# Optimization experiments

Measured on AMD Instinct MI355X. Metric: run time of the kernel, lower is better.

Reference implementation:

```python
import jax, jax.numpy as jnp
import numpy as np

T = 48; S = 48; H = 250; EMB = 300; VOCAB = 50000; NL = 5


def setup_inputs():
    key = jax.random.key(0)
    ks = jax.random.split(key, 32)
    def rn(k, shape, scale=0.05):
        return jax.random.normal(k, shape, dtype=jnp.float32) * scale
    return {
        "x1": jax.random.randint(ks[0], (T,), 0, VOCAB),
        "x2": jax.random.randint(ks[1], (S,), 0, VOCAB),
        "emb": rn(ks[2], (VOCAB, EMB), 1.0),
        "w_ih_f": rn(ks[3], (4 * H, EMB)),
        "w_hh_f": rn(ks[4], (4 * H, H)),
        "b_f": rn(ks[5], (4 * H,)),
        "w_ih_b": rn(ks[6], (4 * H, EMB)),
        "w_hh_b": rn(ks[7], (4 * H, H)),
        "b_b": rn(ks[8], (4 * H,)),
        "c1_w": rn(ks[9], (128, 13, 3, 3)),  "c1_b": rn(ks[10], (128,)),
        "c2_w": rn(ks[11], (164, 128, 3, 3)), "c2_b": rn(ks[12], (164,)),
        "c3_w": rn(ks[13], (192, 164, 3, 3)), "c3_b": rn(ks[14], (192,)),
        "c4_w": rn(ks[15], (192, 192, 3, 3)), "c4_b": rn(ks[16], (192,)),
        "c5_w": rn(ks[17], (128, 192, 3, 3)), "c5_b": rn(ks[18], (128,)),
        "dnn_w": rn(ks[19], (128, 128)), "dnn_b": rn(ks[20], (128,)),
        "out_w": rn(ks[21], (NL, 128)), "out_b": rn(ks[22], (NL,)),
    }


def _lstm_dir(xW, w_hh, b, reverse):
    # xW: [T, 4H] precomputed input projection
    def cell(carry, g_in):
        h, c = carry
        g = g_in + h @ w_hh.T + b
        i, f, gg, o = jnp.split(g, 4)
        i = jax.nn.sigmoid(i); f = jax.nn.sigmoid(f)
        gg = jnp.tanh(gg); o = jax.nn.sigmoid(o)
        c = f * c + i * gg
        h = o * jnp.tanh(c)
        return (h, c), h
    h0 = jnp.zeros((w_hh.shape[1],), xW.dtype)
    _, hs = jax.lax.scan(cell, (h0, h0), xW, reverse=reverse)
    return hs  # [T, H], aligned to input positions


def _bilstm(x, w_ih_f, w_hh_f, b_f, w_ih_b, w_hh_b, b_b):
    hf = _lstm_dir(x @ w_ih_f.T, w_hh_f, b_f, False)
    hb = _lstm_dir(x @ w_ih_b.T, w_hh_b, b_b, True)
    return jnp.stack([hf, hb], axis=1)  # [T, 2, H]


def _sim(a, b):
    # a:[T,D], b:[S,D] -> [3,T,S] channels (dot, cos, l2) -- fully batched
    dot = a @ b.T
    na = jnp.sqrt(jnp.sum(a * a, -1))
    nb = jnp.sqrt(jnp.sum(b * b, -1))
    cos = dot / (na[:, None] * nb[None, :] + 1e-8)
    d2 = jnp.maximum(na[:, None] ** 2 + nb[None, :] ** 2 - 2.0 * dot, 1e-12)
    l2 = jnp.sqrt(d2)
    return jnp.stack([dot, cos, l2], 0)


def _sim_cube(seq1, seq2):
    h1f, h1b = seq1[:, 0], seq1[:, 1]
    h2f, h2b = seq2[:, 0], seq2[:, 1]
    parts = [
        _sim(jnp.concatenate([h1f, h1b], -1), jnp.concatenate([h2f, h2b], -1)),
        _sim(h1f, h2f),
        _sim(h1b, h2b),
        _sim(h1f + h1b, h2f + h2b),
    ]
    pad = jnp.zeros((1, seq1.shape[0], seq2.shape[0]), seq1.dtype)  # channel 12
    return jnp.concatenate(parts + [pad], 0)  # [13, T, S]


def _greedy_select(plane):
    # greedy non-conflicting pair selection over top (T+S) entries
    t, s = plane.shape
    _, idx = jax.lax.top_k(plane.reshape(-1), t + s)
    def step(carry, i):
        s1, s2, m = carry
        p1 = i // t  # faithful to original (divides by len(s1tag))
        p2 = i % s
        ok = (s1[p1] + s2[p2]) == 0
        s1 = s1.at[p1].set(jnp.where(ok, 1, s1[p1]))
        s2 = s2.at[p2].set(jnp.where(ok, 1, s2[p2]))
        m = m.at[p1, p2].set(m[p1, p2] | ok)
        return (s1, s2, m), None
    init = (jnp.zeros(t, jnp.int32), jnp.zeros(s, jnp.int32), jnp.zeros((t, s), bool))
    (_, _, m), _ = jax.lax.scan(step, init, idx)
    return m


def _focus_cube(sc):
    sel = _greedy_select(sc[10]) | _greedy_select(sc[11])
    mask = jnp.where(sel[None], 1.0, 0.1).astype(sc.dtype)  # 0.1 base per VDPWI
    mask = mask.at[12].set(1.0)
    return mask * sc


def _convnet(x, c1_w, c1_b, c2_w, c2_b, c3_w, c3_b, c4_w, c4_b, c5_w, c5_b,
             dnn_w, dnn_b, out_w, out_b):
    def conv(x, w, b):
        y = jax.lax.conv_general_dilated(
            x, w, (1, 1), ((1, 1), (1, 1)),
            dimension_numbers=("NCHW", "OIHW", "NCHW"))
        return y + b[None, :, None, None]
    def pool(x, k, st):
        return jax.lax.reduce_window(
            x, -jnp.inf, jax.lax.max, (1, 1, k, k), (1, 1, st, st), "VALID")
    x = pool(jax.nn.relu(conv(x, c1_w, c1_b)), 2, 2)  # 48->24
    x = pool(jax.nn.relu(conv(x, c2_w, c2_b)), 2, 2)  # 24->12
    x = pool(jax.nn.relu(conv(x, c3_w, c3_b)), 2, 2)  # 12->6
    x = pool(jax.nn.relu(conv(x, c4_w, c4_b)), 2, 2)  # 6->3
    x = pool(jax.nn.relu(conv(x, c5_w, c5_b)), 3, 1)  # 3->1
    x = x.reshape(x.shape[0], -1)  # [1, 128]
    x = jax.nn.relu(x @ dnn_w.T + dnn_b)
    return x @ out_w.T + out_b


def reference(x1, x2, emb, w_ih_f, w_hh_f, b_f, w_ih_b, w_hh_b, b_b,
              c1_w, c1_b, c2_w, c2_b, c3_w, c3_b, c4_w, c4_b, c5_w, c5_b,
              dnn_w, dnn_b, out_w, out_b):
    e1 = emb[x1]  # [T, 300]
    e2 = emb[x2]  # [S, 300]
    seq1 = _bilstm(e1, w_ih_f, w_hh_f, b_f, w_ih_b, w_hh_b, b_b)
    seq2 = _bilstm(e2, w_ih_f, w_hh_f, b_f, w_ih_b, w_hh_b, b_b)
    sc = _sim_cube(seq1, seq2)        # [13, T, S]
    fc = _focus_cube(sc)
    logits = _convnet(fc[None], c1_w, c1_b, c2_w, c2_b, c3_w, c3_b,
                      c4_w, c4_b, c5_w, c5_b, dnn_w, dnn_b, out_w, out_b)
    return jax.nn.log_softmax(logits, axis=-1)
```

## Files before the change

### kernel.cpp

```cpp
#include <hip/hip_runtime.h>
#include <math.h>


typedef __attribute__((ext_vector_type(2))) _Float16 h2f;
typedef unsigned long long u64;

#define OFF_XW    0
#define OFF_HS    192000
#define OFF_SC    240000
#define OFF_BUFA  269952
#define OFF_BUFB  343680
#define OFF_WIHT  367296
#define OFF_WPK   967296
#define OFF_SEL   1217296

__device__ __forceinline__ float sigf(float x) { return 1.f / (1.f + expf(-x)); }

#if __has_builtin(__builtin_amdgcn_fdot2)
__device__ __forceinline__ float dot2(h2f a, h2f b, float c) {
    return __builtin_amdgcn_fdot2(a, b, c, false);
}
#else
__device__ __forceinline__ float dot2(h2f a, h2f b, float c) {
    return c + (float)a.x * (float)b.x + (float)a.y * (float)b.y;
}
#endif

__global__ void transpose_wih_kernel(const float* __restrict__ wf, const float* __restrict__ wb,
                                     float* __restrict__ wT)
{
    __shared__ float tile[32][33];
    int dir = blockIdx.z;
    const float* w = dir ? wb : wf;

    int j = blockIdx.x * 32 + threadIdx.y;
    int k = blockIdx.y * 32 + threadIdx.x;
    if (j < 1000 && k < 300)
        tile[threadIdx.y][threadIdx.x] = w[(size_t)j * 300 + k];
    __syncthreads();

    int ko = blockIdx.y * 32 + threadIdx.y;
    int jo = blockIdx.x * 32 + threadIdx.x;
    if (ko < 300 && jo < 1000)
        wT[(size_t)dir * 300000 + (size_t)ko * 1000 + jo] = tile[threadIdx.x][threadIdx.y];
}

__global__ void pack_whh_kernel(const float* __restrict__ wf, const float* __restrict__ wb,
                                unsigned int* __restrict__ wpk)
{
    int dir = blockIdx.x / 1000;
    int j   = blockIdx.x % 1000;
    const float* w = (dir ? wb : wf) + (size_t)j * 250;
    int p = threadIdx.x;
    if (p < 125) {
        float2 v = *(const float2*)(w + 2 * p);
        h2f pv; pv.x = (_Float16)v.x; pv.y = (_Float16)v.y;
        wpk[(size_t)dir * 125000 + (size_t)p * 1000 + j] = *(unsigned int*)&pv;
    }
}

__global__ void embed_xw_kernel(const int* __restrict__ x1, const int* __restrict__ x2,
                                const float* __restrict__ emb, const float* __restrict__ wT,
                                const float* __restrict__ b_f, const float* __restrict__ b_b,
                                float* __restrict__ xW)
{
    int t = blockIdx.x % 48;
    int m = blockIdx.x / 48;
    const int* x = (m < 2) ? x1 : x2;
    const float* w = wT + (size_t)(m & 1) * 300000;
    const float* bias = (m & 1) ? b_b : b_f;

    __shared__ float e[300];
    int row = x[t];
    for (int k = threadIdx.x; k < 300; k += 512)
        e[k] = emb[(size_t)row * 300 + k];
    __syncthreads();

    int j0 = threadIdx.x;
    int j1 = threadIdx.x + 512;
    int j1c = j1 < 1000 ? j1 : 999;
    float a0 = 0.f, a1 = 0.f;
    #pragma unroll 4
    for (int k = 0; k < 300; ++k) {
        float ek = e[k];
        const float* wr = w + (size_t)k * 1000;
        a0 += ek * wr[j0];
        a1 += ek * wr[j1c];
    }
    float* out = xW + ((size_t)m * 48 + t) * 1000;
    out[j0] = a0 + bias[j0];
    if (j1 < 1000) out[j1] = a1 + bias[j1];
}

__global__ void __launch_bounds__(512, 1) lstm_kernel(
    const float* __restrict__ xW, const unsigned int* __restrict__ wpk,
    float* __restrict__ hs)
{
    int m   = blockIdx.x;
    int dir = m & 1;
    const unsigned int* wp = wpk + (size_t)dir * 125000;
    const float* xw = xW + (size_t)m * 48000;
    float* out      = hs + (size_t)m * 12000;

    int t = threadIdx.x;
    bool active = t < 500;
    int r0 = t, r1 = t + 500;

    __shared__ __align__(16) unsigned int hp[128];
    __shared__ float fo_lds[500];
    __shared__ unsigned int wl[12 * 1000];

    for (int idx = t; idx < 12000; idx += 512)
        wl[idx] = wp[idx];

    h2f w0r[113], w1r[113];
    if (active) {
        #pragma unroll
        for (int p = 0; p < 113; ++p) {
            unsigned int a = wp[(p + 12) * 1000 + r0];
            unsigned int b = wp[(p + 12) * 1000 + r1];
            w0r[p] = *(h2f*)&a;
            w1r[p] = *(h2f*)&b;
        }
    }
    if (t < 128) hp[t] = 0u;
    float c = 0.f;
    __syncthreads();

    for (int step = 0; step < 48; ++step) {
        int tt = dir ? 47 - step : step;
        float a0 = 0.f, a1 = 0.f;
        if (active) {
            const float* xwt = xw + tt * 1000;
            a0 = xwt[r0];
            a1 = xwt[r1];
            const uint4* hp4 = (const uint4*)hp;
            #pragma unroll
            for (int q = 0; q < 3; ++q) {
                uint4 hq = hp4[q];
                h2f h0 = *(h2f*)&hq.x, h1 = *(h2f*)&hq.y, h2v = *(h2f*)&hq.z, h3 = *(h2f*)&hq.w;
                unsigned int u00 = wl[(4 * q + 0) * 1000 + r0], u01 = wl[(4 * q + 0) * 1000 + r1];
                unsigned int u10 = wl[(4 * q + 1) * 1000 + r0], u11 = wl[(4 * q + 1) * 1000 + r1];
                unsigned int u20 = wl[(4 * q + 2) * 1000 + r0], u21 = wl[(4 * q + 2) * 1000 + r1];
                unsigned int u30 = wl[(4 * q + 3) * 1000 + r0], u31 = wl[(4 * q + 3) * 1000 + r1];
                a0 = dot2(*(h2f*)&u00, h0, a0);  a1 = dot2(*(h2f*)&u01, h0, a1);
                a0 = dot2(*(h2f*)&u10, h1, a0);  a1 = dot2(*(h2f*)&u11, h1, a1);
                a0 = dot2(*(h2f*)&u20, h2v, a0); a1 = dot2(*(h2f*)&u21, h2v, a1);
                a0 = dot2(*(h2f*)&u30, h3, a0);  a1 = dot2(*(h2f*)&u31, h3, a1);
            }
            #pragma unroll
            for (int jj = 3; jj < 31; ++jj) {
                uint4 hq = hp4[jj];
                h2f h0 = *(h2f*)&hq.x, h1 = *(h2f*)&hq.y, h2v = *(h2f*)&hq.z, h3 = *(h2f*)&hq.w;
                int p = 4 * jj - 12;
                a0 = dot2(w0r[p + 0], h0, a0);  a1 = dot2(w1r[p + 0], h0, a1);
                a0 = dot2(w0r[p + 1], h1, a0);  a1 = dot2(w1r[p + 1], h1, a1);
                a0 = dot2(w0r[p + 2], h2v, a0); a1 = dot2(w1r[p + 2], h2v, a1);
                a0 = dot2(w0r[p + 3], h3, a0);  a1 = dot2(w1r[p + 3], h3, a1);
            }
            {
                unsigned int hq = hp[124];
                h2f hv = *(h2f*)&hq;
                a0 = dot2(w0r[112], hv, a0);
                a1 = dot2(w1r[112], hv, a1);
            }
            if (t >= 250) {
                fo_lds[t - 250] = sigf(a0);
                fo_lds[250 + (t - 250)] = sigf(a1);
            }
        }
        __syncthreads();
        if (t < 250) {
            float iv = sigf(a0);
            float gv = tanhf(a1);
            float fv = fo_lds[t];
            float ov = fo_lds[250 + t];
            c = fv * c + iv * gv;
            float hn = ov * tanhf(c);
            out[tt * 250 + t] = hn;
            float hi = __shfl_down(hn, 1);
            if (!(t & 1)) {
                h2f pv; pv.x = (_Float16)hn; pv.y = (_Float16)hi;
                hp[t >> 1] = *(unsigned int*)&pv;
            }
        }
        __syncthreads();
    }
}

__global__ void sim_kernel(const float* __restrict__ hs, float* __restrict__ sc)
{
    int p = blockIdx.x;
    int i = p / 48, jj = p % 48;
    const float* h1f = hs + ((size_t)0 * 48 + i) * 250;
    const float* h1b = hs + ((size_t)1 * 48 + i) * 250;
    const float* h2f = hs + ((size_t)2 * 48 + jj) * 250;
    const float* h2b = hs + ((size_t)3 * 48 + jj) * 250;
    int lane = threadIdx.x;
    float dff = 0.f, dbb = 0.f, dfb = 0.f, dbf = 0.f;
    float sfa = 0.f, sba = 0.f, caa = 0.f;
    float sfb = 0.f, sbb = 0.f, cbb = 0.f;
    for (int k = lane; k < 250; k += 64) {
        float af = h1f[k], ab = h1b[k], bf = h2f[k], bb = h2b[k];
        dff += af * bf; dbb += ab * bb; dfb += af * bb; dbf += ab * bf;
        sfa += af * af; sba += ab * ab; caa += af * ab;
        sfb += bf * bf; sbb += bb * bb; cbb += bf * bb;
    }
    #pragma unroll
    for (int o = 32; o; o >>= 1) {
        dff += __shfl_down(dff, o); dbb += __shfl_down(dbb, o);
        dfb += __shfl_down(dfb, o); dbf += __shfl_down(dbf, o);
        sfa += __shfl_down(sfa, o); sba += __shfl_down(sba, o);
        caa += __shfl_down(caa, o);
        sfb += __shfl_down(sfb, o); sbb += __shfl_down(sbb, o);
        cbb += __shfl_down(cbb, o);
    }
    if (lane == 0) {
        #define EMIT(basep, dotv, sa2, sb2)                                 \
        {                                                                   \
            float na = sqrtf(sa2), nbv = sqrtf(sb2);                        \
            float dv = (dotv);                                              \
            sc[(basep) * 2304 + p] = dv;                                    \
            sc[((basep) + 1) * 2304 + p] = dv / (na * nbv + 1e-8f);         \
            float d2 = fmaxf(na * na + nbv * nbv - 2.f * dv, 1e-12f);       \
            sc[((basep) + 2) * 2304 + p] = sqrtf(d2);                       \
        }
        EMIT(0, dff + dbb, sfa + sba, sfb + sbb);
        EMIT(3, dff, sfa, sfb);
        EMIT(6, dbb, sba, sbb);
        EMIT(9, dff + dfb + dbf + dbb, sfa + sba + 2.f * caa, sfb + sbb + 2.f * cbb);
        #undef EMIT
    }
}

__global__ void greedy_kernel(const float* __restrict__ sc, unsigned char* __restrict__ sel)
{
    __shared__ unsigned char selL[2304];
    int lane = threadIdx.x;
    int plane = 10 + blockIdx.x;

    u64 v[36];
    #pragma unroll
    for (int q = 0; q < 36; ++q) {
        int i = lane + 64 * q;
        unsigned int u = __float_as_uint(sc[plane * 2304 + i]);
        unsigned int ord = (u & 0x80000000u) ? ~u : (u | 0x80000000u);
        v[q] = ((u64)ord << 32) | (unsigned int)(4095 - i);
        selL[i] = 0;
    }

    #pragma unroll
    for (int a = 0; a < 35; ++a) {
        #pragma unroll
        for (int b = 0; b < 35 - a; ++b) {
            u64 lo = v[b] < v[b + 1] ? v[b] : v[b + 1];
            u64 hi = v[b] < v[b + 1] ? v[b + 1] : v[b];
            v[b] = hi; v[b + 1] = lo;
        }
    }
    __syncthreads();

    u64 m1 = 0, m2 = 0;
    for (int it = 0; it < 96; ++it) {
        u64 bv = v[0];
        #pragma unroll
        for (int o = 1; o < 64; o <<= 1) {
            u64 ov = __shfl_xor(bv, o);
            if (ov > bv) bv = ov;
        }
        int idx = 4095 - (int)(bv & 0xFFFFFFFFu);
        int p1 = idx / 48, p2 = idx % 48;
        bool ok = !((m1 >> p1) & 1) && !((m2 >> p2) & 1);
        if (ok) { m1 |= 1ull << p1; m2 |= 1ull << p2; }
        if (v[0] == bv) {
            if (ok) selL[idx] = 1;
            #pragma unroll
            for (int q = 0; q < 35; ++q) v[q] = v[q + 1];
            v[35] = 0;
        }
    }
    __syncthreads();
    for (int q = 0; q < 36; ++q) {
        int i = lane + 64 * q;
        sel[blockIdx.x * 2304 + i] = selL[i];
    }
}

__global__ void conv1_pool_kernel(const float* __restrict__ sc, const unsigned char* __restrict__ sel,
                                  const float* __restrict__ w, const float* __restrict__ bias,
                                  float* __restrict__ out)
{
    __shared__ float tile[256];
    int co  = blockIdx.x / 9;
    int tl  = blockIdx.x % 9;
    int ty0 = (tl / 3) * 16, tx0 = (tl % 3) * 16;
    int tx = threadIdx.x % 16, ty = threadIdx.x / 16;
    int x = tx0 + tx, y = ty0 + ty;

    float mv[9];
    #pragma unroll
    for (int ky = 0; ky < 3; ++ky) {
        int iy = y + ky - 1;
        #pragma unroll
        for (int kx = 0; kx < 3; ++kx) {
            int ix = x + kx - 1;
            float mm = 0.f;
            if (iy >= 0 && iy < 48 && ix >= 0 && ix < 48) {
                int p = iy * 48 + ix;
                mm = (sel[p] | sel[2304 + p]) ? 1.0f : 0.1f;
            }
            mv[ky * 3 + kx] = mm;
        }
    }

    float acc = bias[co];
    const float* wco = w + (size_t)co * 13 * 9;
    for (int ci = 0; ci < 12; ++ci) {
        const float* inp = sc + (size_t)ci * 2304;
        const float* wp = wco + ci * 9;
        #pragma unroll
        for (int ky = 0; ky < 3; ++ky) {
            int iy = y + ky - 1;
            if (iy < 0 || iy >= 48) continue;
            #pragma unroll
            for (int kx = 0; kx < 3; ++kx) {
                int ix = x + kx - 1;
                if (ix < 0 || ix >= 48) continue;
                acc += inp[iy * 48 + ix] * mv[ky * 3 + kx] * wp[ky * 3 + kx];
            }
        }
    }
    tile[threadIdx.x] = acc > 0.f ? acc : 0.f;
    __syncthreads();
    if (threadIdx.x < 64) {
        int py = threadIdx.x / 8, px = threadIdx.x % 8;
        float a = tile[(py * 2) * 16 + px * 2];
        float b = tile[(py * 2) * 16 + px * 2 + 1];
        float cc = tile[(py * 2 + 1) * 16 + px * 2];
        float d = tile[(py * 2 + 1) * 16 + px * 2 + 1];
        float best = fmaxf(fmaxf(a, b), fmaxf(cc, d));
        out[(size_t)co * 576 + (ty0 / 2 + py) * 24 + (tx0 / 2 + px)] = best;
    }
}

__global__ void conv_cs_kernel(const float* __restrict__ in, const float* __restrict__ w,
                               const float* __restrict__ bias, float* __restrict__ out,
                               int Cin, int H, int W, int tileH, int tileW,
                               int cpc, int CC, int pk, int ps, int PHf, int PWf)
{
    extern __shared__ float sm[];
    int P = tileH * tileW;
    int co = blockIdx.x;
    int ty0 = blockIdx.y * tileH, tx0 = blockIdx.z * tileW;
    int t = threadIdx.x;
    int pix = t % P, chunk = t / P;
    int y = ty0 + pix / tileW, x = tx0 + pix % tileW;
    int c0 = chunk * cpc;
    int c1 = c0 + cpc; if (c1 > Cin) c1 = Cin;

    float acc = 0.f;
    const float* wco = w + (size_t)co * Cin * 9;
    for (int ci = c0; ci < c1; ++ci) {
        const float* inp = in + (size_t)ci * H * W;
        const float* wp = wco + (size_t)ci * 9;
        #pragma unroll
        for (int ky = 0; ky < 3; ++ky) {
            int iy = y + ky - 1;
            if (iy < 0 || iy >= H) continue;
            const float* rowp = inp + iy * W;
            #pragma unroll
            for (int kx = 0; kx < 3; ++kx) {
                int ix = x + kx - 1;
                if (ix < 0 || ix >= W) continue;
                acc += rowp[ix] * wp[ky * 3 + kx];
            }
        }
    }
    sm[t] = acc;
    __syncthreads();
    float* res = sm + P * CC;
    if (chunk == 0) {
        float tot = bias[co];
        for (int cc2 = 0; cc2 < CC; ++cc2) tot += sm[pix + cc2 * P];
        res[pix] = tot > 0.f ? tot : 0.f;
    }
    __syncthreads();
    int pH = (tileH - pk) / ps + 1, pW = (tileW - pk) / ps + 1;
    if (t < pH * pW) {
        int py = t / pW, px = t % pW;
        float best = -INFINITY;
        for (int dy = 0; dy < pk; ++dy)
            for (int dx = 0; dx < pk; ++dx) {
                float v = res[(py * ps + dy) * tileW + (px * ps + dx)];
                best = v > best ? v : best;
            }
        out[((size_t)co * PHf + (ty0 / ps + py)) * PWf + (tx0 / ps + px)] = best;
    }
}

__global__ void head_kernel(const float* __restrict__ feat,
                            const float* __restrict__ dnn_w, const float* __restrict__ dnn_b,
                            const float* __restrict__ out_w, const float* __restrict__ out_b,
                            float* __restrict__ out)
{
    __shared__ float y[128];
    __shared__ float logits[5];
    int j = threadIdx.x;
    float acc = dnn_b[j];
    for (int k = 0; k < 128; ++k) acc += feat[k] * dnn_w[j * 128 + k];
    y[j] = acc > 0.f ? acc : 0.f;
    __syncthreads();
    if (j < 5) {
        float a = out_b[j];
        for (int k = 0; k < 128; ++k) a += y[k] * out_w[j * 128 + k];
        logits[j] = a;
    }
    __syncthreads();
    if (j == 0) {
        float m = logits[0];
        for (int l = 1; l < 5; ++l) m = fmaxf(m, logits[l]);
        float s = 0.f;
        for (int l = 0; l < 5; ++l) s += expf(logits[l] - m);
        float lse = logf(s);
        for (int l = 0; l < 5; ++l) out[l] = logits[l] - m - lse;
    }
}

extern "C" void kernel_launch(void* const* d_in, const int* in_sizes, int n_in,
                              void* d_out, int out_size, void* d_ws, size_t ws_size,
                              hipStream_t stream)
{
    const int*   x1     = (const int*)d_in[0];
    const int*   x2     = (const int*)d_in[1];
    const float* emb    = (const float*)d_in[2];
    const float* w_ih_f = (const float*)d_in[3];
    const float* w_hh_f = (const float*)d_in[4];
    const float* b_f    = (const float*)d_in[5];
    const float* w_ih_b = (const float*)d_in[6];
    const float* w_hh_b = (const float*)d_in[7];
    const float* b_b    = (const float*)d_in[8];
    const float* c1_w   = (const float*)d_in[9];
    const float* c1_b   = (const float*)d_in[10];
    const float* c2_w   = (const float*)d_in[11];
    const float* c2_b   = (const float*)d_in[12];
    const float* c3_w   = (const float*)d_in[13];
    const float* c3_b   = (const float*)d_in[14];
    const float* c4_w   = (const float*)d_in[15];
    const float* c4_b   = (const float*)d_in[16];
    const float* c5_w   = (const float*)d_in[17];
    const float* c5_b   = (const float*)d_in[18];
    const float* dnn_w  = (const float*)d_in[19];
    const float* dnn_b  = (const float*)d_in[20];
    const float* out_w  = (const float*)d_in[21];
    const float* out_b  = (const float*)d_in[22];

    float* ws    = (float*)d_ws;
    float* xW    = ws + OFF_XW;
    float* hsb   = ws + OFF_HS;
    float* sc    = ws + OFF_SC;
    float* bufA  = ws + OFF_BUFA;
    float* bufB  = ws + OFF_BUFB;
    float* wihT  = ws + OFF_WIHT;
    unsigned int* wpk = (unsigned int*)(ws + OFF_WPK);
    unsigned char* sel = (unsigned char*)(ws + OFF_SEL);
    float* outp  = (float*)d_out;

    transpose_wih_kernel<<<dim3(32, 10, 2), dim3(32, 32), 0, stream>>>(w_ih_f, w_ih_b, wihT);
    pack_whh_kernel<<<2000, 128, 0, stream>>>(w_hh_f, w_hh_b, wpk);
    embed_xw_kernel<<<192, 512, 0, stream>>>(x1, x2, emb, wihT, b_f, b_b, xW);
    lstm_kernel<<<4, 512, 0, stream>>>(xW, wpk, hsb);
    sim_kernel<<<2304, 64, 0, stream>>>(hsb, sc);
    greedy_kernel<<<2, 64, 0, stream>>>(sc, sel);

    conv1_pool_kernel<<<128 * 9, 256, 0, stream>>>(sc, sel, c1_w, c1_b, bufA);
    conv_cs_kernel<<<dim3(164, 2, 2), 576, (576 + 144) * 4, stream>>>(
        bufA, c2_w, c2_b, bufB, 128, 24, 24, 12, 12, 32, 4, 2, 2, 12, 12);
    conv_cs_kernel<<<dim3(192, 1, 1), 576, (576 + 144) * 4, stream>>>(
        bufB, c3_w, c3_b, bufA, 164, 12, 12, 12, 12, 41, 4, 2, 2, 6, 6);
    conv_cs_kernel<<<dim3(192, 1, 1), 576, (576 + 36) * 4, stream>>>(
        bufA, c4_w, c4_b, bufB, 192, 6, 6, 6, 6, 12, 16, 2, 2, 3, 3);
    conv_cs_kernel<<<dim3(128, 1, 1), 576, (576 + 9) * 4, stream>>>(
        bufB, c5_w, c5_b, bufA, 192, 3, 3, 3, 3, 3, 64, 3, 1, 1, 1);

    head_kernel<<<1, 128, 0, stream>>>(bufA, dnn_w, dnn_b, out_w, out_b, outp);
}
```

Before: 348.4 us.

## Merge weight-prep kernels, fuse conv5 with head, prefetch LSTM inputs

Merges the two weight-preparation kernels into one launch and fuses the last conv layer, its pooling and the dense head into a single 1024-thread block, removing two kernel launches. Inside the LSTM it stores the LDS-resident recurrent weights as uint4 so each row takes one wide LDS read, and it prefetches the next timestep's input projection during the current step. The fused conv5 runs on a single block and may be slower than the 128-block version, and the prefetch adds registers to an already register-heavy kernel.

Measured after the change: 516.1 us. 1.48x slower.

```diff
diff --git a/kernel.cpp b/kernel.cpp
--- a/kernel.cpp
+++ b/kernel.cpp
@@ -26,36 +26,38 @@
 }
 #endif
 
-__global__ void transpose_wih_kernel(const float* __restrict__ wf, const float* __restrict__ wb,
-                                     float* __restrict__ wT)
-{
-    __shared__ float tile[32][33];
-    int dir = blockIdx.z;
-    const float* w = dir ? wb : wf;
-
-    int j = blockIdx.x * 32 + threadIdx.y;
-    int k = blockIdx.y * 32 + threadIdx.x;
-    if (j < 1000 && k < 300)
-        tile[threadIdx.y][threadIdx.x] = w[(size_t)j * 300 + k];
-    __syncthreads();
-
-    int ko = blockIdx.y * 32 + threadIdx.y;
-    int jo = blockIdx.x * 32 + threadIdx.x;
-    if (ko < 300 && jo < 1000)
-        wT[(size_t)dir * 300000 + (size_t)ko * 1000 + jo] = tile[threadIdx.x][threadIdx.y];
-}
-
-__global__ void pack_whh_kernel(const float* __restrict__ wf, const float* __restrict__ wb,
-                                unsigned int* __restrict__ wpk)
-{
-    int dir = blockIdx.x / 1000;
-    int j   = blockIdx.x % 1000;
-    const float* w = (dir ? wb : wf) + (size_t)j * 250;
-    int p = threadIdx.x;
-    if (p < 125) {
-        float2 v = *(const float2*)(w + 2 * p);
-        h2f pv; pv.x = (_Float16)v.x; pv.y = (_Float16)v.y;
-        wpk[(size_t)dir * 125000 + (size_t)p * 1000 + j] = *(unsigned int*)&pv;
+__global__ void prep_kernel(const float* __restrict__ wihf, const float* __restrict__ wihb,
+                            const float* __restrict__ whhf, const float* __restrict__ whhb,
+                            float* __restrict__ wT, unsigned int* __restrict__ wpk)
+{
+    if (blockIdx.z < 2) {
+        __shared__ float tile[32][33];
+        int dir = blockIdx.z;
+        const float* w = dir ? wihb : wihf;
+
+        int j = blockIdx.x * 32 + threadIdx.y;
+        int k = blockIdx.y * 32 + threadIdx.x;
+        if (j < 1000 && k < 300)
+            tile[threadIdx.y][threadIdx.x] = w[(size_t)j * 300 + k];
+        __syncthreads();
+
+        int ko = blockIdx.y * 32 + threadIdx.y;
+        int jo = blockIdx.x * 32 + threadIdx.x;
+        if (ko < 300 && jo < 1000)
+            wT[(size_t)dir * 300000 + (size_t)ko * 1000 + jo] = tile[threadIdx.x][threadIdx.y];
+    } else {
+        int tid = threadIdx.y * 32 + threadIdx.x;
+        int flat = (blockIdx.x * 10 + blockIdx.y) * 1024 + tid;
+        if (flat < 250000) {
+            int dir = flat / 125000;
+            int rem = flat % 125000;
+            int j = rem / 125;
+            int p = rem % 125;
+            const float* w = (dir ? whhb : whhf) + (size_t)j * 250;
+            float2 v = *(const float2*)(w + 2 * p);
+            h2f pv; pv.x = (_Float16)v.x; pv.y = (_Float16)v.y;
+            wpk[(size_t)dir * 125000 + (size_t)p * 1000 + j] = *(unsigned int*)&pv;
+        }
     }
 }
 
@@ -108,10 +110,17 @@
 
     __shared__ __align__(16) unsigned int hp[128];
     __shared__ float fo_lds[500];
-    __shared__ unsigned int wl[12 * 1000];
-
-    for (int idx = t; idx < 12000; idx += 512)
-        wl[idx] = wp[idx];
+    __shared__ __align__(16) uint4 wl4[3 * 1000];
+
+    for (int idx = t; idx < 3000; idx += 512) {
+        int q = idx / 1000, r = idx % 1000;
+        uint4 v;
+        v.x = wp[(4 * q + 0) * 1000 + r];
+        v.y = wp[(4 * q + 1) * 1000 + r];
+        v.z = wp[(4 * q + 2) * 1000 + r];
+        v.w = wp[(4 * q + 3) * 1000 + r];
+        wl4[idx] = v;
+    }
 
     h2f w0r[113], w1r[113];
     if (active) {
@@ -125,28 +134,37 @@
     }
     if (t < 128) hp[t] = 0u;
     float c = 0.f;
+
+    int tt = dir ? 47 : 0;
+    float px0 = 0.f, px1 = 0.f;
+    if (active) {
+        px0 = xw[tt * 1000 + r0];
+        px1 = xw[tt * 1000 + r1];
+    }
     __syncthreads();
 
     for (int step = 0; step < 48; ++step) {
-        int tt = dir ? 47 - step : step;
+        int ttn = dir ? 46 - step : step + 1;
+        float n0 = 0.f, n1 = 0.f;
+        if (active && step < 47) {
+            n0 = xw[ttn * 1000 + r0];
+            n1 = xw[ttn * 1000 + r1];
+        }
         float a0 = 0.f, a1 = 0.f;
         if (active) {
-            const float* xwt = xw + tt * 1000;
-            a0 = xwt[r0];
-            a1 = xwt[r1];
+            a0 = px0;
+            a1 = px1;
             const uint4* hp4 = (const uint4*)hp;
             #pragma unroll
             for (int q = 0; q < 3; ++q) {
                 uint4 hq = hp4[q];
                 h2f h0 = *(h2f*)&hq.x, h1 = *(h2f*)&hq.y, h2v = *(h2f*)&hq.z, h3 = *(h2f*)&hq.w;
-                unsigned int u00 = wl[(4 * q + 0) * 1000 + r0], u01 = wl[(4 * q + 0) * 1000 + r1];
-                unsigned int u10 = wl[(4 * q + 1) * 1000 + r0], u11 = wl[(4 * q + 1) * 1000 + r1];
-                unsigned int u20 = wl[(4 * q + 2) * 1000 + r0], u21 = wl[(4 * q + 2) * 1000 + r1];
-                unsigned int u30 = wl[(4 * q + 3) * 1000 + r0], u31 = wl[(4 * q + 3) * 1000 + r1];
-                a0 = dot2(*(h2f*)&u00, h0, a0);  a1 = dot2(*(h2f*)&u01, h0, a1);
-                a0 = dot2(*(h2f*)&u10, h1, a0);  a1 = dot2(*(h2f*)&u11, h1, a1);
-                a0 = dot2(*(h2f*)&u20, h2v, a0); a1 = dot2(*(h2f*)&u21, h2v, a1);
-                a0 = dot2(*(h2f*)&u30, h3, a0);  a1 = dot2(*(h2f*)&u31, h3, a1);
+                uint4 wv0 = wl4[q * 1000 + r0];
+                uint4 wv1 = wl4[q * 1000 + r1];
+                a0 = dot2(*(h2f*)&wv0.x, h0, a0);  a1 = dot2(*(h2f*)&wv1.x, h0, a1);
+                a0 = dot2(*(h2f*)&wv0.y, h1, a0);  a1 = dot2(*(h2f*)&wv1.y, h1, a1);
+                a0 = dot2(*(h2f*)&wv0.z, h2v, a0); a1 = dot2(*(h2f*)&wv1.z, h2v, a1);
+                a0 = dot2(*(h2f*)&wv0.w, h3, a0);  a1 = dot2(*(h2f*)&wv1.w, h3, a1);
             }
             #pragma unroll
             for (int jj = 3; jj < 31; ++jj) {
@@ -184,6 +202,7 @@
                 hp[t >> 1] = *(unsigned int*)&pv;
             }
         }
+        px0 = n0; px1 = n1; tt = ttn;
         __syncthreads();
     }
 }
@@ -398,31 +417,84 @@
     }
 }
 
-__global__ void head_kernel(const float* __restrict__ feat,
-                            const float* __restrict__ dnn_w, const float* __restrict__ dnn_b,
-                            const float* __restrict__ out_w, const float* __restrict__ out_b,
-                            float* __restrict__ out)
-{
-    __shared__ float y[128];
+__global__ void __launch_bounds__(1024) conv5_head_kernel(
+    const float* __restrict__ in,
+    const float* __restrict__ c5_w, const float* __restrict__ c5_b,
+    const float* __restrict__ dnn_w, const float* __restrict__ dnn_b,
+    const float* __restrict__ out_w, const float* __restrict__ out_b,
+    float* __restrict__ out)
+{
+    __shared__ float part[128 * 8 * 9];
+    __shared__ float feat[128];
+    __shared__ float yv[128];
     __shared__ float logits[5];
-    int j = threadIdx.x;
-    float acc = dnn_b[j];
-    for (int k = 0; k < 128; ++k) acc += feat[k] * dnn_w[j * 128 + k];
-    y[j] = acc > 0.f ? acc : 0.f;
-    __syncthreads();
-    if (j < 5) {
-        float a = out_b[j];
-        for (int k = 0; k < 128; ++k) a += y[k] * out_w[j * 128 + k];
-        logits[j] = a;
-    }
-    __syncthreads();
-    if (j == 0) {
-        float m = logits[0];
-        for (int l = 1; l < 5; ++l) m = fmaxf(m, logits[l]);
-        float s = 0.f;
-        for (int l = 0; l < 5; ++l) s += expf(logits[l] - m);
-        float lse = logf(s);
-        for (int l = 0; l < 5; ++l) out[l] = logits[l] - m - lse;
+
+    int t = threadIdx.x;
+    int co = t >> 3, s = t & 7;
+
+    float acc[9];
+    #pragma unroll
+    for (int p = 0; p < 9; ++p) acc[p] = 0.f;
+
+    const float* wco = c5_w + (size_t)co * 192 * 9;
+    for (int ci = s * 24; ci < s * 24 + 24; ++ci) {
+        const float* inp = in + (size_t)ci * 9;
+        const float* wp = wco + (size_t)ci * 9;
+        #pragma unroll
+        for (int p = 0; p < 9; ++p) {
+            int y0 = p / 3, x0 = p % 3;
+            float a = 0.f;
+            #pragma unroll
+            for (int ky = 0; ky < 3; ++ky) {
+                int iy = y0 + ky - 1;
+                if (iy < 0 || iy >= 3) continue;
+                #pragma unroll
+                for (int kx = 0; kx < 3; ++kx) {
+                    int ix = x0 + kx - 1;
+                    if (ix < 0 || ix >= 3) continue;
+                    a += inp[iy * 3 + ix] * wp[ky * 3 + kx];
+                }
+            }
+            acc[p] += a;
+        }
+    }
+    #pragma unroll
+    for (int p = 0; p < 9; ++p) part[(co * 8 + s) * 9 + p] = acc[p];
+    __syncthreads();
+
+    if (s == 0) {
+        float best = -INFINITY;
+        #pragma unroll
+        for (int p = 0; p < 9; ++p) {
+            float v = c5_b[co];
+            #pragma unroll
+            for (int ss = 0; ss < 8; ++ss) v += part[(co * 8 + ss) * 9 + p];
+            v = v > 0.f ? v : 0.f;
+            best = v > best ? v : best;
+        }
+        feat[co] = best;
+    }
+    __syncthreads();
+
+    if (t < 128) {
+        float a = dnn_b[t];
+        for (int k = 0; k < 128; ++k) a += feat[k] * dnn_w[t * 128 + k];
+        yv[t] = a > 0.f ? a : 0.f;
+    }
+    __syncthreads();
+    if (t < 5) {
+        float a = out_b[t];
+        for (int k = 0; k < 128; ++k) a += yv[k] * out_w[t * 128 + k];
+        logits[t] = a;
+    }
+    __syncthreads();
+    if (t == 0) {
+        float mx = logits[0];
+        for (int l = 1; l < 5; ++l) mx = fmaxf(mx, logits[l]);
+        float sum = 0.f;
+        for (int l = 0; l < 5; ++l) sum += expf(logits[l] - mx);
+        float lse = logf(sum);
+        for (int l = 0; l < 5; ++l) out[l] = logits[l] - mx - lse;
     }
 }
 
@@ -465,8 +537,8 @@
     unsigned char* sel = (unsigned char*)(ws + OFF_SEL);
     float* outp  = (float*)d_out;
 
-    transpose_wih_kernel<<<dim3(32, 10, 2), dim3(32, 32), 0, stream>>>(w_ih_f, w_ih_b, wihT);
-    pack_whh_kernel<<<2000, 128, 0, stream>>>(w_hh_f, w_hh_b, wpk);
+    prep_kernel<<<dim3(32, 10, 3), dim3(32, 32), 0, stream>>>(
+        w_ih_f, w_ih_b, w_hh_f, w_hh_b, wihT, wpk);
     embed_xw_kernel<<<192, 512, 0, stream>>>(x1, x2, emb, wihT, b_f, b_b, xW);
     lstm_kernel<<<4, 512, 0, stream>>>(xW, wpk, hsb);
     sim_kernel<<<2304, 64, 0, stream>>>(hsb, sc);
@@ -479,8 +551,6 @@
         bufB, c3_w, c3_b, bufA, 164, 12, 12, 12, 12, 41, 4, 2, 2, 6, 6);
     conv_cs_kernel<<<dim3(192, 1, 1), 576, (576 + 36) * 4, stream>>>(
         bufA, c4_w, c4_b, bufB, 192, 6, 6, 6, 6, 12, 16, 2, 2, 3, 3);
-    conv_cs_kernel<<<dim3(128, 1, 1), 576, (576 + 9) * 4, stream>>>(
-        bufB, c5_w, c5_b, bufA, 192, 3, 3, 3, 3, 3, 64, 3, 1, 1, 1);
-
-    head_kernel<<<1, 128, 0, stream>>>(bufA, dnn_w, dnn_b, out_w, out_b, outp);
-}
+    conv5_head_kernel<<<1, 1024, 0, stream>>>(
+        bufB, c5_w, c5_b, dnn_w, dnn_b, out_w, out_b, outp);
+}
```
